# Kernel tuning notes

Measured on AMD Instinct MI355X. Metric: run time of the kernel, lower is better.

The kernel has to match this reference:

```python
import jax, jax.numpy as jnp
import numpy as np

B, T, D, K = 8, 4096, 512, 4  # batch, seq, dims, num_types
TOP = 2  # default num=2 in weights()


def setup_inputs() -> dict:
    key = jax.random.key(0)
    ks = jax.random.split(key, 6)
    return {
        "m0": jax.random.normal(ks[0], (B, T, D), dtype=jnp.float32),
        "m1": jax.random.normal(ks[1], (B, T, D), dtype=jnp.float32),
        "m2": jax.random.normal(ks[2], (B, T, D), dtype=jnp.float32),
        "m3": jax.random.normal(ks[3], (B, T, D), dtype=jnp.float32),
        "W_top": jax.random.normal(ks[4], (K, D * K), dtype=jnp.float32) * 0.02,
        "b_top": jnp.zeros((K,), dtype=jnp.float32),
        "W_soft": jax.random.normal(ks[5], (K, D * K), dtype=jnp.float32) * 0.02,
        "b_soft": jnp.zeros((K,), dtype=jnp.float32),
        "alpha": jnp.ones((1,), dtype=jnp.float32),
    }


def reference(m0, m1, m2, m3, W_top, b_top, W_soft, b_soft, alpha):
    stack = jnp.stack([m0, m1, m2, m3], axis=-1)            # [B,T,D,K]
    x = stack.reshape(stack.shape[0], stack.shape[1], -1)    # [B,T,D*K]
    logits = x @ W_top.T + b_top                             # [B,T,K]
    vals, idx = jax.lax.top_k(logits, TOP)                   # [B,T,TOP]
    # scatter softmax(topk vals) back into a zeros-[B,T,K] hard routing
    hard = jnp.einsum(
        "btnk,btn->btk",
        jax.nn.one_hot(idx, K, dtype=logits.dtype),
        jax.nn.softmax(vals, axis=-1),
    )
    soft = jax.nn.softmax(x @ W_soft.T + b_soft, axis=-1)    # [B,T,K]
    a = jax.nn.sigmoid(alpha)                                # [1], broadcasts
    w = a * hard + (1.0 - a) * soft                          # [B,T,K]
    return jnp.sum(stack * w[:, :, None, :], axis=-1)        # [B,T,D]
```

## Files before the change

kernel.cpp:

```cpp
#include <hip/hip_runtime.h>
#include <math.h>

#define TOKENS (8 * 4096)
#define DDIM 512
#define TPB 256
#define NBLK 512
#define WAVES_PER_BLK (TPB / 64)

__global__ __launch_bounds__(TPB)
__attribute__((amdgpu_waves_per_eu(2, 2)))
void router_kernel(
    const float* __restrict__ m0, const float* __restrict__ m1,
    const float* __restrict__ m2, const float* __restrict__ m3,
    const float* __restrict__ W_top, const float* __restrict__ b_top,
    const float* __restrict__ W_soft, const float* __restrict__ b_soft,
    const float* __restrict__ alpha, float* __restrict__ out)
{
    __shared__ float lt[16 * DDIM];
    __shared__ float ls[16 * DDIM];

    const int tid = threadIdx.x;

    for (int n = tid; n < 8192; n += TPB) {
        int j = n >> 11;
        int e = n & 2047;
        int d = e >> 2;
        int k = e & 3;
        int c = d >> 8;
        int dl = d & 255;
        int dst = ((((k << 1) + c) << 2) + j) * 256 + dl;
        lt[dst] = W_top[n];
        ls[dst] = W_soft[n];
    }

    const float bt0 = b_top[0], bt1 = b_top[1], bt2 = b_top[2], bt3 = b_top[3];
    const float bs0 = b_soft[0], bs1 = b_soft[1], bs2 = b_soft[2], bs3 = b_soft[3];
    const float a = 1.0f / (1.0f + __expf(-alpha[0]));
    const float na = 1.0f - a;

    __syncthreads();

    const int lane = tid & 63;
    const int wv = tid >> 6;
    const int gw = blockIdx.x * WAVES_PER_BLK + wv;
    const int stride = NBLK * WAVES_PER_BLK * 2;

    const float* __restrict__ ms[4] = {m0, m1, m2, m3};

    for (int t0 = gw * 2; t0 < TOKENS; t0 += stride) {
        float accT[2][4] = {{0, 0, 0, 0}, {0, 0, 0, 0}};
        float accS[2][4] = {{0, 0, 0, 0}, {0, 0, 0, 0}};
        #pragma unroll
        for (int k = 0; k < 4; ++k) {
            #pragma unroll
            for (int c = 0; c < 2; ++c) {
                const int goff = t0 * DDIM + (c << 8) + (lane << 2);
                const float4 a0 = *(const float4*)(ms[k] + goff);
                const float4 a1 = *(const float4*)(ms[k] + goff + DDIM);
                const int segbase = (((k << 1) + c) << 10) + (lane << 2);
                #pragma unroll
                for (int j = 0; j < 4; ++j) {
                    const float4 wt = *(const float4*)&lt[segbase + (j << 8)];
                    const float4 ws = *(const float4*)&ls[segbase + (j << 8)];
                    accT[0][j] += a0.x * wt.x + a0.y * wt.y + a0.z * wt.z + a0.w * wt.w;
                    accT[1][j] += a1.x * wt.x + a1.y * wt.y + a1.z * wt.z + a1.w * wt.w;
                    accS[0][j] += a0.x * ws.x + a0.y * ws.y + a0.z * ws.z + a0.w * ws.w;
                    accS[1][j] += a1.x * ws.x + a1.y * ws.y + a1.z * ws.z + a1.w * ws.w;
                }
            }
        }

        #pragma unroll
        for (int tk = 0; tk < 2; ++tk) {
            #pragma unroll
            for (int j = 0; j < 4; ++j) {
                float vt = accT[tk][j];
                float vs = accS[tk][j];
                #pragma unroll
                for (int m = 1; m < 64; m <<= 1) {
                    vt += __shfl_xor(vt, m, 64);
                    vs += __shfl_xor(vs, m, 64);
                }
                accT[tk][j] = vt;
                accS[tk][j] = vs;
            }
        }

        #pragma unroll
        for (int tk = 0; tk < 2; ++tk) {
            const float l0 = accT[tk][0] + bt0, l1 = accT[tk][1] + bt1;
            const float l2 = accT[tk][2] + bt2, l3 = accT[tk][3] + bt3;

            int i1 = 0; float v1 = l0;
            if (l1 > v1) { v1 = l1; i1 = 1; }
            if (l2 > v1) { v1 = l2; i1 = 2; }
            if (l3 > v1) { v1 = l3; i1 = 3; }
            float v2 = -INFINITY; int i2 = 0;
            if (i1 != 0)            { v2 = l0; i2 = 0; }
            if (i1 != 1 && l1 > v2) { v2 = l1; i2 = 1; }
            if (i1 != 2 && l2 > v2) { v2 = l2; i2 = 2; }
            if (i1 != 3 && l3 > v2) { v2 = l3; i2 = 3; }

            const float eh = __expf(v2 - v1);
            const float p1 = 1.0f / (1.0f + eh);
            const float p2 = eh * p1;

            const float x0 = accS[tk][0] + bs0, x1 = accS[tk][1] + bs1;
            const float x2 = accS[tk][2] + bs2, x3 = accS[tk][3] + bs3;
            const float mx = fmaxf(fmaxf(x0, x1), fmaxf(x2, x3));
            const float e0 = __expf(x0 - mx), e1 = __expf(x1 - mx);
            const float e2 = __expf(x2 - mx), e3 = __expf(x3 - mx);
            const float inv = 1.0f / (e0 + e1 + e2 + e3);

            float w0 = na * e0 * inv;
            float w1 = na * e1 * inv;
            float w2 = na * e2 * inv;
            float w3 = na * e3 * inv;
            const float ap1 = a * p1, ap2 = a * p2;
            w0 += (i1 == 0 ? ap1 : 0.0f) + (i2 == 0 ? ap2 : 0.0f);
            w1 += (i1 == 1 ? ap1 : 0.0f) + (i2 == 1 ? ap2 : 0.0f);
            w2 += (i1 == 2 ? ap1 : 0.0f) + (i2 == 2 ? ap2 : 0.0f);
            w3 += (i1 == 3 ? ap1 : 0.0f) + (i2 == 3 ? ap2 : 0.0f);

            const int base = (t0 + tk) * DDIM + (lane << 2);
            #pragma unroll
            for (int c = 0; c < 2; ++c) {
                const float4 r0 = *(const float4*)(m0 + base + (c << 8));
                const float4 r1 = *(const float4*)(m1 + base + (c << 8));
                const float4 r2 = *(const float4*)(m2 + base + (c << 8));
                const float4 r3 = *(const float4*)(m3 + base + (c << 8));
                float4 o;
                o.x = r0.x * w0 + r1.x * w1 + r2.x * w2 + r3.x * w3;
                o.y = r0.y * w0 + r1.y * w1 + r2.y * w2 + r3.y * w3;
                o.z = r0.z * w0 + r1.z * w1 + r2.z * w2 + r3.z * w3;
                o.w = r0.w * w0 + r1.w * w1 + r2.w * w2 + r3.w * w3;
                *(float4*)(out + base + (c << 8)) = o;
            }
        }
    }
}

extern "C" void kernel_launch(void* const* d_in, const int* in_sizes, int n_in,
                              void* d_out, int out_size, void* d_ws, size_t ws_size,
                              hipStream_t stream) {
    const float* m0     = (const float*)d_in[0];
    const float* m1     = (const float*)d_in[1];
    const float* m2     = (const float*)d_in[2];
    const float* m3     = (const float*)d_in[3];
    const float* W_top  = (const float*)d_in[4];
    const float* b_top  = (const float*)d_in[5];
    const float* W_soft = (const float*)d_in[6];
    const float* b_soft = (const float*)d_in[7];
    const float* alpha  = (const float*)d_in[8];
    float* outp = (float*)d_out;

    router_kernel<<<NBLK, TPB, 0, stream>>>(m0, m1, m2, m3, W_top, b_top,
                                            W_soft, b_soft, alpha, outp);
}
```

Before: 369.5 us.

## Keep token inputs in registers for reuse, use nontemporal I/O, raise occupancy

Each wave now processes one token per iteration and holds the 4x2 float4 input vectors in registers. The second pass that re-read m0..m3 from global memory for the weighted sum is gone, so the 32 KB per-token-pair reload no longer happens. Loads and stores use nontemporal builtins to avoid polluting cache, and the block size and waves-per-EU are doubled to raise occupancy. The risk is less ILP per wave from dropping the two-token unroll, plus higher register pressure at the forced occupancy.

```diff
diff --git a/kernel.cpp b/kernel.cpp
--- a/kernel.cpp
+++ b/kernel.cpp
@@ -3,12 +3,14 @@
 
 #define TOKENS (8 * 4096)
 #define DDIM 512
-#define TPB 256
+#define TPB 512
 #define NBLK 512
 #define WAVES_PER_BLK (TPB / 64)
 
+typedef float v4f __attribute__((ext_vector_type(4)));
+
 __global__ __launch_bounds__(TPB)
-__attribute__((amdgpu_waves_per_eu(2, 2)))
+__attribute__((amdgpu_waves_per_eu(4, 4)))
 void router_kernel(
     const float* __restrict__ m0, const float* __restrict__ m1,
     const float* __restrict__ m2, const float* __restrict__ m3,
@@ -43,99 +45,92 @@
     const int lane = tid & 63;
     const int wv = tid >> 6;
     const int gw = blockIdx.x * WAVES_PER_BLK + wv;
-    const int stride = NBLK * WAVES_PER_BLK * 2;
+    const int stride = NBLK * WAVES_PER_BLK;
 
     const float* __restrict__ ms[4] = {m0, m1, m2, m3};
 
-    for (int t0 = gw * 2; t0 < TOKENS; t0 += stride) {
-        float accT[2][4] = {{0, 0, 0, 0}, {0, 0, 0, 0}};
-        float accS[2][4] = {{0, 0, 0, 0}, {0, 0, 0, 0}};
+    for (int t = gw; t < TOKENS; t += stride) {
+        const int gbase = t * DDIM + (lane << 2);
+
+        v4f r[4][2];
         #pragma unroll
         for (int k = 0; k < 4; ++k) {
             #pragma unroll
             for (int c = 0; c < 2; ++c) {
-                const int goff = t0 * DDIM + (c << 8) + (lane << 2);
-                const float4 a0 = *(const float4*)(ms[k] + goff);
-                const float4 a1 = *(const float4*)(ms[k] + goff + DDIM);
+                r[k][c] = __builtin_nontemporal_load(
+                    (const v4f*)(ms[k] + gbase + (c << 8)));
+            }
+        }
+
+        float accT[4] = {0.f, 0.f, 0.f, 0.f};
+        float accS[4] = {0.f, 0.f, 0.f, 0.f};
+        #pragma unroll
+        for (int k = 0; k < 4; ++k) {
+            #pragma unroll
+            for (int c = 0; c < 2; ++c) {
+                const v4f a0 = r[k][c];
                 const int segbase = (((k << 1) + c) << 10) + (lane << 2);
                 #pragma unroll
                 for (int j = 0; j < 4; ++j) {
-                    const float4 wt = *(const float4*)&lt[segbase + (j << 8)];
-                    const float4 ws = *(const float4*)&ls[segbase + (j << 8)];
-                    accT[0][j] += a0.x * wt.x + a0.y * wt.y + a0.z * wt.z + a0.w * wt.w;
-                    accT[1][j] += a1.x * wt.x + a1.y * wt.y + a1.z * wt.z + a1.w * wt.w;
-                    accS[0][j] += a0.x * ws.x + a0.y * ws.y + a0.z * ws.z + a0.w * ws.w;
-                    accS[1][j] += a1.x * ws.x + a1.y * ws.y + a1.z * ws.z + a1.w * ws.w;
+                    const v4f wt = *(const v4f*)&lt[segbase + (j << 8)];
+                    const v4f ws = *(const v4f*)&ls[segbase + (j << 8)];
+                    accT[j] += a0.x * wt.x + a0.y * wt.y + a0.z * wt.z + a0.w * wt.w;
+                    accS[j] += a0.x * ws.x + a0.y * ws.y + a0.z * ws.z + a0.w * ws.w;
                 }
             }
         }
 
         #pragma unroll
-        for (int tk = 0; tk < 2; ++tk) {
+        for (int j = 0; j < 4; ++j) {
+            float vt = accT[j];
+            float vs = accS[j];
             #pragma unroll
-            for (int j = 0; j < 4; ++j) {
-                float vt = accT[tk][j];
-                float vs = accS[tk][j];
-                #pragma unroll
-                for (int m = 1; m < 64; m <<= 1) {
-                    vt += __shfl_xor(vt, m, 64);
-                    vs += __shfl_xor(vs, m, 64);
-                }
-                accT[tk][j] = vt;
-                accS[tk][j] = vs;
+            for (int mm = 1; mm < 64; mm <<= 1) {
+                vt += __shfl_xor(vt, mm, 64);
+                vs += __shfl_xor(vs, mm, 64);
             }
+            accT[j] = vt;
+            accS[j] = vs;
         }
 
+        const float l0 = accT[0] + bt0, l1 = accT[1] + bt1;
+        const float l2 = accT[2] + bt2, l3 = accT[3] + bt3;
+
+        int i1 = 0; float v1 = l0;
+        if (l1 > v1) { v1 = l1; i1 = 1; }
+        if (l2 > v1) { v1 = l2; i1 = 2; }
+        if (l3 > v1) { v1 = l3; i1 = 3; }
+        float v2 = -INFINITY; int i2 = 0;
+        if (i1 != 0)            { v2 = l0; i2 = 0; }
+        if (i1 != 1 && l1 > v2) { v2 = l1; i2 = 1; }
+        if (i1 != 2 && l2 > v2) { v2 = l2; i2 = 2; }
+        if (i1 != 3 && l3 > v2) { v2 = l3; i2 = 3; }
+
+        const float eh = __expf(v2 - v1);
+        const float p1 = 1.0f / (1.0f + eh);
+        const float p2 = eh * p1;
+
+        const float x0 = accS[0] + bs0, x1 = accS[1] + bs1;
+        const float x2 = accS[2] + bs2, x3 = accS[3] + bs3;
+        const float mx = fmaxf(fmaxf(x0, x1), fmaxf(x2, x3));
+        const float e0 = __expf(x0 - mx), e1 = __expf(x1 - mx);
+        const float e2 = __expf(x2 - mx), e3 = __expf(x3 - mx);
+        const float inv = 1.0f / (e0 + e1 + e2 + e3);
+
+        float w0 = na * e0 * inv;
+        float w1 = na * e1 * inv;
+        float w2 = na * e2 * inv;
+        float w3 = na * e3 * inv;
+        const float ap1 = a * p1, ap2 = a * p2;
+        w0 += (i1 == 0 ? ap1 : 0.0f) + (i2 == 0 ? ap2 : 0.0f);
+        w1 += (i1 == 1 ? ap1 : 0.0f) + (i2 == 1 ? ap2 : 0.0f);
+        w2 += (i1 == 2 ? ap1 : 0.0f) + (i2 == 2 ? ap2 : 0.0f);
+        w3 += (i1 == 3 ? ap1 : 0.0f) + (i2 == 3 ? ap2 : 0.0f);
+
         #pragma unroll
-        for (int tk = 0; tk < 2; ++tk) {
-            const float l0 = accT[tk][0] + bt0, l1 = accT[tk][1] + bt1;
-            const float l2 = accT[tk][2] + bt2, l3 = accT[tk][3] + bt3;
-
-            int i1 = 0; float v1 = l0;
-            if (l1 > v1) { v1 = l1; i1 = 1; }
-            if (l2 > v1) { v1 = l2; i1 = 2; }
-            if (l3 > v1) { v1 = l3; i1 = 3; }
-            float v2 = -INFINITY; int i2 = 0;
-            if (i1 != 0)            { v2 = l0; i2 = 0; }
-            if (i1 != 1 && l1 > v2) { v2 = l1; i2 = 1; }
-            if (i1 != 2 && l2 > v2) { v2 = l2; i2 = 2; }
-            if (i1 != 3 && l3 > v2) { v2 = l3; i2 = 3; }
-
-            const float eh = __expf(v2 - v1);
-            const float p1 = 1.0f / (1.0f + eh);
-            const float p2 = eh * p1;
-
-            const float x0 = accS[tk][0] + bs0, x1 = accS[tk][1] + bs1;
-            const float x2 = accS[tk][2] + bs2, x3 = accS[tk][3] + bs3;
-            const float mx = fmaxf(fmaxf(x0, x1), fmaxf(x2, x3));
-            const float e0 = __expf(x0 - mx), e1 = __expf(x1 - mx);
-            const float e2 = __expf(x2 - mx), e3 = __expf(x3 - mx);
-            const float inv = 1.0f / (e0 + e1 + e2 + e3);
-
-            float w0 = na * e0 * inv;
-            float w1 = na * e1 * inv;
-            float w2 = na * e2 * inv;
-            float w3 = na * e3 * inv;
-            const float ap1 = a * p1, ap2 = a * p2;
-            w0 += (i1 == 0 ? ap1 : 0.0f) + (i2 == 0 ? ap2 : 0.0f);
-            w1 += (i1 == 1 ? ap1 : 0.0f) + (i2 == 1 ? ap2 : 0.0f);
-            w2 += (i1 == 2 ? ap1 : 0.0f) + (i2 == 2 ? ap2 : 0.0f);
-            w3 += (i1 == 3 ? ap1 : 0.0f) + (i2 == 3 ? ap2 : 0.0f);
-
-            const int base = (t0 + tk) * DDIM + (lane << 2);
-            #pragma unroll
-            for (int c = 0; c < 2; ++c) {
-                const float4 r0 = *(const float4*)(m0 + base + (c << 8));
-                const float4 r1 = *(const float4*)(m1 + base + (c << 8));
-                const float4 r2 = *(const float4*)(m2 + base + (c << 8));
-                const float4 r3 = *(const float4*)(m3 + base + (c << 8));
-                float4 o;
-                o.x = r0.x * w0 + r1.x * w1 + r2.x * w2 + r3.x * w3;
-                o.y = r0.y * w0 + r1.y * w1 + r2.y * w2 + r3.y * w3;
-                o.z = r0.z * w0 + r1.z * w1 + r2.z * w2 + r3.z * w3;
-                o.w = r0.w * w0 + r1.w * w1 + r2.w * w2 + r3.w * w3;
-                *(float4*)(out + base + (c << 8)) = o;
-            }
+        for (int c = 0; c < 2; ++c) {
+            v4f o = r[0][c] * w0 + r[1][c] * w1 + r[2][c] * w2 + r[3][c] * w3;
+            __builtin_nontemporal_store(o, (v4f*)(out + gbase + (c << 8)));
         }
     }
 }
```

New measurement: 567.2 us. 1.54x slower.
